# Kernel optimization log

Measured on AMD Instinct MI355X. Metric: run time of the kernel, lower is better.

The kernel has to match this reference:

```python
import jax, jax.numpy as jnp
import numpy as np

WS = 7  # window_size
HEADS = 12
HEAD_DIM = 32
HIDDEN = 384
INNER = HEADS * HEAD_DIM


def _relative_position_index(ws):
    coords = np.stack(np.meshgrid(np.arange(ws), np.arange(ws), indexing='ij'))  # (2, ws, ws)
    flat = coords.reshape(2, -1)  # (2, ws*ws)
    rel = flat[:, :, None] - flat[:, None, :]  # (2, N, N)
    rel = rel.transpose(1, 2, 0).copy()
    rel[:, :, 0] += ws - 1
    rel[:, :, 1] += ws - 1
    rel[:, :, 0] *= 2 * ws - 1
    return rel.sum(-1)  # (N, N) int


def setup_inputs() -> dict:
    key = jax.random.key(0)
    k1, k2, k3, k4, k5 = jax.random.split(key, 5)
    x = jax.random.normal(k1, (32, 56, 56, HIDDEN), dtype=jnp.float32)
    w_qkv = jax.random.normal(k2, (HIDDEN, INNER * 3), dtype=jnp.float32) * (HIDDEN ** -0.5)
    w_out = jax.random.normal(k3, (INNER, HIDDEN), dtype=jnp.float32) * (INNER ** -0.5)
    b_out = jax.random.normal(k4, (HIDDEN,), dtype=jnp.float32) * 0.02
    bias_table = jax.random.normal(k5, ((2 * WS - 1) * (2 * WS - 1), HEADS), dtype=jnp.float32) * 0.02
    return {"x": x, "w_qkv": w_qkv, "w_out": w_out, "b_out": b_out, "bias_table": bias_table}


def _window_attention(x, w_qkv, w_out, b_out, bias_table):
    b, n_h, n_w, _ = x.shape
    ws, h, d = WS, HEADS, HEAD_DIM
    nw_h, nw_w = n_h // ws, n_w // ws
    N = ws * ws

    qkv = x @ w_qkv  # (b, n_h, n_w, 3*inner)
    q, k, v = jnp.split(qkv, 3, axis=-1)

    def to_windows(t):
        # (b, n_h, n_w, h*d) -> (b, h, nw_h*nw_w, ws*ws, d)
        t = t.reshape(b, nw_h, ws, nw_w, ws, h, d)
        t = t.transpose(0, 5, 1, 3, 2, 4, 6)
        return t.reshape(b, h, nw_h * nw_w, N, d)

    q, k, v = map(to_windows, (q, k, v))
    scale = d ** -0.5
    dots = jnp.einsum('bhwid,bhwjd->bhwij', q, k) * scale
    attn = jax.nn.softmax(dots, axis=-1)

    rel_idx = jnp.asarray(_relative_position_index(ws))  # (N, N)
    bias = bias_table[rel_idx.reshape(-1)].reshape(N, N, h)  # gather
    bias = bias.transpose(2, 0, 1)  # (h, N, N)
    # NOTE: faithful to source — bias added AFTER softmax
    attn = attn + bias[None, :, None, :, :]

    out = jnp.einsum('bhwij,bhwjd->bhwid', attn, v)  # (b, h, nw, N, d)
    out = out.reshape(b, h, nw_h, nw_w, ws, ws, d)
    out = out.transpose(0, 2, 4, 3, 5, 1, 6).reshape(b, n_h, n_w, h * d)
    return out @ w_out + b_out


def reference(x, w_qkv, w_out, b_out, bias_table):
    return _window_attention(x, w_qkv, w_out, b_out, bias_table)
```

## Files before the change

### kernel.cpp

```cpp
#include <hip/hip_runtime.h>
#include <hip/hip_bf16.h>
#include <cstdint>

#define TOK 100352
#define HID 384
#define NQKV 1152
#define NHEADS 12
#define HDIM 32

typedef __attribute__((ext_vector_type(8))) short bhalf8;
typedef __attribute__((ext_vector_type(4))) float f32x4;

__device__ __forceinline__ ushort f2bf(float f) {
  uint32_t u = __float_as_uint(f);
  return (ushort)((u + 0x7FFFu + ((u >> 16) & 1u)) >> 16);
}

__device__ __forceinline__ void gload_lds16(const ushort* g, ushort* l) {
  __builtin_amdgcn_global_load_lds(
      (const __attribute__((address_space(1))) unsigned int*)g,
      (__attribute__((address_space(3))) unsigned int*)l, 16, 0, 0);
}

__device__ __forceinline__ uint32_t cvtpk(float a, float b) {
  uint32_t r;
  asm("v_cvt_pk_bf16_f32 %0, %1, %2" : "=v"(r) : "v"(a), "v"(b));
  return r;
}

__global__ __launch_bounds__(256)
void cvt_bf16(const float* __restrict__ in, ushort* __restrict__ out, const int n8) {
  const int i = blockIdx.x * 256 + threadIdx.x;
  if (i >= n8) return;
  const float4 f0 = ((const float4*)in)[(size_t)i * 2];
  const float4 f1 = ((const float4*)in)[(size_t)i * 2 + 1];
  bhalf8 v;
  v[0] = (short)f2bf(f0.x); v[1] = (short)f2bf(f0.y);
  v[2] = (short)f2bf(f0.z); v[3] = (short)f2bf(f0.w);
  v[4] = (short)f2bf(f1.x); v[5] = (short)f2bf(f1.y);
  v[6] = (short)f2bf(f1.z); v[7] = (short)f2bf(f1.w);
  ((bhalf8*)out)[i] = v;
}

__global__ __launch_bounds__(256)
void transpose_cvt(const float* __restrict__ in, ushort* __restrict__ out,
                   const int R, const int C) {
  const int i = blockIdx.x * 256 + threadIdx.x;
  if (i >= R * C) return;
  const int r = i % R, c = i / R;
  out[i] = f2bf(in[(size_t)r * C + c]);
}

__global__ __launch_bounds__(256)
void expand_bias_pad(const float* __restrict__ bt, float* __restrict__ bx) {
  const int i = blockIdx.x * 256 + threadIdx.x;
  if (i >= NHEADS * 49 * 64) return;
  const int head = i / (49 * 64);
  const int rem = i % (49 * 64);
  const int q = rem / 64, k = rem % 64;
  float v = 0.f;
  if (k < 49) {
    const int idx = (q / 7 - k / 7 + 6) * 13 + (q % 7 - k % 7 + 6);
    v = bt[idx * NHEADS + head];
  }
  bx[i] = v;
}

template<bool OUT_F32_BIAS>
__global__ __launch_bounds__(256)
void gemm_bt(const ushort* __restrict__ A, const ushort* __restrict__ Bt,
             const float* __restrict__ bias, void* __restrict__ Cp,
             const int N, const int K, const int nbx)
{
  __shared__ ushort As[128 * 64];
  __shared__ ushort Bs[128 * 64];

  const int tid = threadIdx.x;
  const int lane = tid & 63;
  const int wave = tid >> 6;
  const int wm = wave >> 1, wn = wave & 1;
  const int l15 = lane & 15, l16 = lane >> 4;

  int bid = blockIdx.x;
  const int nwg = gridDim.x;
  if ((nwg & 7) == 0) bid = (bid & 7) * (nwg >> 3) + (bid >> 3);
  const int row0 = (bid / nbx) * 128;
  const int col0 = (bid % nbx) * 128;

  f32x4 acc[4][4] = {};

  for (int ko = 0; ko < K; ko += 64) {
    if (ko) __syncthreads();
    #pragma unroll
    for (int it = 0; it < 4; ++it) {
      const int chunk = it * 4 + wave;
      const int idx = chunk * 64 + lane;
      const int m = idx >> 3;
      const int k8 = (((idx & 7) ^ (m & 7)) * 8);
      gload_lds16(A + (size_t)(row0 + m) * K + ko + k8, &As[chunk * 512]);
      gload_lds16(Bt + (size_t)(col0 + m) * K + ko + k8, &Bs[chunk * 512]);
    }
    __syncthreads();
    #pragma unroll
    for (int kk = 0; kk < 64; kk += 32) {
      bhalf8 af[4], bfr[4];
      #pragma unroll
      for (int f = 0; f < 4; ++f) {
        const int ra = wm * 64 + f * 16 + l15;
        const int rb = wn * 64 + f * 16 + l15;
        const int kb = (kk + l16 * 8) * 2;
        af[f]  = *(const bhalf8*)((const char*)As + ra * 128 + (kb ^ ((ra & 7) << 4)));
        bfr[f] = *(const bhalf8*)((const char*)Bs + rb * 128 + (kb ^ ((rb & 7) << 4)));
      }
      #pragma unroll
      for (int fm = 0; fm < 4; ++fm)
        #pragma unroll
        for (int fn = 0; fn < 4; ++fn)
          acc[fm][fn] = __builtin_amdgcn_mfma_f32_16x16x32_bf16(af[fm], bfr[fn], acc[fm][fn], 0, 0, 0);
    }
  }

  #pragma unroll
  for (int fm = 0; fm < 4; ++fm) {
    const int rb = row0 + wm * 64 + fm * 16 + l16 * 4;
    #pragma unroll
    for (int fn = 0; fn < 4; ++fn) {
      const int cc = col0 + wn * 64 + fn * 16 + l15;
      const float badd = OUT_F32_BIAS ? bias[cc] : 0.f;
      #pragma unroll
      for (int i = 0; i < 4; ++i) {
        const float vv = acc[fm][fn][i] + badd;
        if (OUT_F32_BIAS) ((float*)Cp)[(size_t)(rb + i) * N + cc] = vv;
        else ((ushort*)Cp)[(size_t)(rb + i) * N + cc] = f2bf(vv);
      }
    }
  }
}

__global__ __launch_bounds__(256)
void win_attn4(const ushort* __restrict__ qkv, const float* __restrict__ biasx,
               ushort* __restrict__ attn_out)
{
  __shared__ ushort VtAll[4][32 * 64];
  __shared__ ushort PsAll[4][64 * 64];

  const int tid = threadIdx.x;
  const int lane = tid & 63, wave = tid >> 6;
  const int l15 = lane & 15, l16 = lane >> 4;
  const int gid = blockIdx.x * 4 + wave;
  const int head = gid % NHEADS;
  const int win = gid / NHEADS;
  const int b = win >> 6, wi = (win >> 3) & 7, wj = win & 7;
  char* Vt = (char*)VtAll[wave];
  char* Ps = (char*)PsAll[wave];

  const int base_row = b * 3136 + wi * 7 * 56 + wj * 7;

  #pragma unroll
  for (int it = 0; it < 4; ++it) {
    const int t = lane;
    const int d0 = it * 8;
    bhalf8 v = {0, 0, 0, 0, 0, 0, 0, 0};
    if (t < 49) {
      const size_t off = (size_t)(base_row + (t / 7) * 56 + (t % 7)) * NQKV
                         + 768 + head * HDIM + d0;
      v = *(const bhalf8*)(qkv + off);
    }
    #pragma unroll
    for (int j = 0; j < 8; ++j) {
      const int d = d0 + j;
      const int byteoff = ((d * 64 + t) * 2) ^ ((d & 7) << 4);
      *(ushort*)(Vt + byteoff) = (ushort)v[j];
    }
  }

  bhalf8 qf[4], kf[4];
  #pragma unroll
  for (int f = 0; f < 4; ++f) {
    const int r = f * 16 + l15;
    const int rr = r < 49 ? r : 48;
    const size_t off = (size_t)(base_row + (rr / 7) * 56 + (rr % 7)) * NQKV
                       + head * HDIM + l16 * 8;
    qf[f] = *(const bhalf8*)(qkv + off);
    kf[f] = *(const bhalf8*)(qkv + off + 384);
  }

  const f32x4 fz = {};
  f32x4 s[4][4];
  __builtin_amdgcn_s_setprio(1);
  #pragma unroll
  for (int fm = 0; fm < 4; ++fm)
    #pragma unroll
    for (int fn = 0; fn < 4; ++fn)
      s[fm][fn] = __builtin_amdgcn_mfma_f32_16x16x32_bf16(kf[fm], qf[fn], fz, 0, 0, 0);
  __builtin_amdgcn_s_setprio(0);

  const float scale = 0.17677669529663687f;
  const float* bq = biasx + (size_t)head * (49 * 64);

  #pragma unroll
  for (int fn = 0; fn < 4; ++fn) {
    const int q = fn * 16 + l15;
    const int xr = (q & 7) << 4;
    char* prow = Ps + q * 128;
    if (fn == 3 && l15 != 0) {
      #pragma unroll
      for (int fm = 0; fm < 4; ++fm) {
        const int b0 = (fm * 16 + l16 * 4) * 2;
        *(uint32_t*)(prow + (b0 ^ xr)) = 0u;
        *(uint32_t*)(prow + (b0 ^ xr) + 4) = 0u;
      }
    } else {
      float e[4][4];
      float local = 0.f;
      #pragma unroll
      for (int fm = 0; fm < 3; ++fm)
        #pragma unroll
        for (int i = 0; i < 4; ++i) {
          e[fm][i] = __expf(s[fm][fn][i] * scale);
          local += e[fm][i];
        }
      e[3][0] = e[3][1] = e[3][2] = e[3][3] = 0.f;
      if (l16 == 0) {
        e[3][0] = __expf(s[3][fn][0] * scale);
        local += e[3][0];
      }
      float sum = local + __shfl_xor(local, 16);
      sum += __shfl_xor(sum, 32);
      const float inv = __builtin_amdgcn_rcpf(sum);
      const float* b4p = bq + q * 64;
      #pragma unroll
      for (int fm = 0; fm < 4; ++fm) {
        const int k0 = fm * 16 + l16 * 4;
        const float4 b4 = *(const float4*)(b4p + k0);
        const uint32_t w0 = cvtpk(fmaf(e[fm][0], inv, b4.x),
                                  fmaf(e[fm][1], inv, b4.y));
        const uint32_t w1 = cvtpk(fmaf(e[fm][2], inv, b4.z),
                                  fmaf(e[fm][3], inv, b4.w));
        const int b0 = (k0 * 2) ^ xr;
        *(uint32_t*)(prow + b0) = w0;
        *(uint32_t*)(prow + b0 + 4) = w1;
      }
    }
  }

  f32x4 o[4][2] = {};
  #pragma unroll
  for (int kk = 0; kk < 64; kk += 32) {
    bhalf8 pf[4], vf[2];
    #pragma unroll
    for (int f = 0; f < 4; ++f) {
      const int r = f * 16 + l15;
      pf[f] = *(const bhalf8*)(Ps + (((r * 64 + kk + l16 * 8) * 2) ^ ((r & 7) << 4)));
    }
    #pragma unroll
    for (int f = 0; f < 2; ++f) {
      const int d = f * 16 + l15;
      vf[f] = *(const bhalf8*)(Vt + (((d * 64 + kk + l16 * 8) * 2) ^ ((d & 7) << 4)));
    }
    __builtin_amdgcn_s_setprio(1);
    #pragma unroll
    for (int fm = 0; fm < 4; ++fm)
      #pragma unroll
      for (int fn = 0; fn < 2; ++fn)
        o[fm][fn] = __builtin_amdgcn_mfma_f32_16x16x32_bf16(pf[fm], vf[fn], o[fm][fn], 0, 0, 0);
    __builtin_amdgcn_s_setprio(0);
  }

  #pragma unroll
  for (int fm = 0; fm < 4; ++fm) {
    #pragma unroll
    for (int i = 0; i < 4; ++i) {
      const int r = fm * 16 + l16 * 4 + i;
      if (r < 49) {
        const int grow = base_row + (r / 7) * 56 + (r % 7);
        #pragma unroll
        for (int fn = 0; fn < 2; ++fn) {
          const int d = fn * 16 + l15;
          attn_out[(size_t)grow * HID + head * HDIM + d] = f2bf(o[fm][fn][i]);
        }
      }
    }
  }
}

extern "C" void kernel_launch(void* const* d_in, const int* in_sizes, int n_in,
                              void* d_out, int out_size, void* d_ws, size_t ws_size,
                              hipStream_t stream) {
  const float* x          = (const float*)d_in[0];
  const float* w_qkv      = (const float*)d_in[1];
  const float* w_out      = (const float*)d_in[2];
  const float* b_out      = (const float*)d_in[3];
  const float* bias_table = (const float*)d_in[4];
  float* out = (float*)d_out;

  ushort* xb     = (ushort*)d_ws;
  ushort* qkv    = xb + (size_t)TOK * HID;
  ushort* wqkvT  = qkv + (size_t)TOK * NQKV;
  ushort* woutT  = wqkvT + (size_t)NQKV * HID;
  float*  biasx  = (float*)(woutT + (size_t)HID * HID);
  ushort* attn_o = xb;

  {
    const int n8 = TOK * HID / 8;
    cvt_bf16<<<dim3((n8 + 255) / 256), dim3(256), 0, stream>>>(x, xb, n8);
    transpose_cvt<<<dim3(HID * NQKV / 256), dim3(256), 0, stream>>>(w_qkv, wqkvT, HID, NQKV);
    transpose_cvt<<<dim3(HID * HID / 256), dim3(256), 0, stream>>>(w_out, woutT, HID, HID);
    expand_bias_pad<<<dim3((NHEADS * 49 * 64 + 255) / 256), dim3(256), 0, stream>>>(
        bias_table, biasx);
  }

  gemm_bt<false><<<dim3((NQKV / 128) * (TOK / 128)), dim3(256), 0, stream>>>(
      xb, wqkvT, nullptr, qkv, NQKV, HID, NQKV / 128);

  win_attn4<<<dim3(2048 * NHEADS / 4), dim3(256), 0, stream>>>(qkv, biasx, attn_o);

  gemm_bt<true><<<dim3((HID / 128) * (TOK / 128)), dim3(256), 0, stream>>>(
      attn_o, woutT, b_out, out, HID, HID, HID / 128);
}
```

Baseline: 342.8 us.

## Replace QKV GEMM with 256x128-tile ping-pong pipelined kernel

Adds a dedicated QKV projection kernel that uses 512 threads and 256x128 output tiles. It triple-buffers A and double-buffers B in LDS using direct global-to-LDS loads with XOR swizzle, and interleaves prefetch issue with MFMA phases separated by barriers and priority hints. The goal is to hide global load latency and raise MFMA utilisation compared with the generic 128x128 gemm. In exchange it uses more LDS and registers per block, which may lower occupancy, and its hand-placed waitcnt logic is fragile.

Result: slower. 370.8 us (+8.1%).

```diff
diff --git a/kernel.cpp b/kernel.cpp
--- a/kernel.cpp
+++ b/kernel.cpp
@@ -66,6 +66,146 @@
   bx[i] = v;
 }
 
+__global__ __launch_bounds__(512)
+void gemm1_ph(const ushort* __restrict__ A, const ushort* __restrict__ Bt,
+              ushort* __restrict__ C)
+{
+  __shared__ ushort AL[3][16384];
+  __shared__ ushort BL[2][8192];
+
+  const int tid = threadIdx.x;
+  const int lane = tid & 63, wave = tid >> 6;
+  const int wr = wave >> 1;
+  const int wc = wave & 1;
+  const int l15 = lane & 15, l16 = lane >> 4;
+
+  int bid = blockIdx.x;
+  const int nwg = gridDim.x;
+  bid = (bid & 7) * (nwg >> 3) + (bid >> 3);
+  const int row0 = (bid / 9) * 256;
+  const int col0 = (bid % 9) * 128;
+
+  f32x4 acc[4][4] = {};
+
+  auto issueA = [&](int buf, int ko, int r) {
+    const int idx = r * 512 + tid;
+    const int m = idx >> 3;
+    const int k8 = ((idx & 7) ^ (m & 7)) * 8;
+    gload_lds16(A + (size_t)(row0 + m) * HID + ko + k8,
+                &AL[buf][r * 4096 + wave * 512]);
+  };
+  auto issueB = [&](int buf, int ko, int r) {
+    const int idx = r * 512 + tid;
+    const int m = idx >> 3;
+    const int k8 = ((idx & 7) ^ (m & 7)) * 8;
+    gload_lds16(Bt + (size_t)(col0 + m) * HID + ko + k8,
+                &BL[buf][r * 4096 + wave * 512]);
+  };
+  auto rdA = [&](const ushort* base, int f, int kk) -> bhalf8 {
+    const int ra = wr * 64 + f * 16 + l15;
+    const int kb = (kk + l16 * 8) * 2;
+    return *(const bhalf8*)((const char*)base + ra * 128 + (kb ^ ((ra & 7) << 4)));
+  };
+  auto rdB = [&](const ushort* base, int f, int kk) -> bhalf8 {
+    const int rb = wc * 64 + f * 16 + l15;
+    const int kb = (kk + l16 * 8) * 2;
+    return *(const bhalf8*)((const char*)base + rb * 128 + (kb ^ ((rb & 7) << 4)));
+  };
+
+  const int nt = HID / 64;
+  #pragma unroll
+  for (int r = 0; r < 4; ++r) issueA(0, 0, r);
+  issueB(0, 0, 0); issueB(0, 0, 1);
+  #pragma unroll
+  for (int r = 0; r < 4; ++r) issueA(1, 64, r);
+  asm volatile("s_waitcnt vmcnt(4)" ::: "memory");
+  __builtin_amdgcn_sched_barrier(0);
+  __builtin_amdgcn_s_barrier();
+
+  for (int t = 0; t < nt; ++t) {
+    const ushort* pA = AL[t % 3];
+    const ushort* pB = BL[t & 1];
+    const int abuf = (t + 2) % 3, bbuf = (t + 1) & 1;
+    const bool preA = (t + 2) < nt, preB = (t + 1) < nt;
+    const int koA = (t + 2) * 64, koB = (t + 1) * 64;
+    bhalf8 a0, a1, a2, a3, bfr[4];
+
+    a0 = rdA(pA, 0, 0); a1 = rdA(pA, 1, 0);
+    bfr[0] = rdB(pB, 0, 0); bfr[1] = rdB(pB, 1, 0);
+    bfr[2] = rdB(pB, 2, 0); bfr[3] = rdB(pB, 3, 0);
+    if (preB) { issueB(bbuf, koB, 0); issueB(bbuf, koB, 1); }
+    __builtin_amdgcn_s_barrier();
+    asm volatile("s_waitcnt lgkmcnt(0)" ::: "memory");
+    __builtin_amdgcn_sched_barrier(0);
+    __builtin_amdgcn_s_setprio(1);
+    #pragma unroll
+    for (int fn = 0; fn < 4; ++fn) {
+      acc[0][fn] = __builtin_amdgcn_mfma_f32_16x16x32_bf16(a0, bfr[fn], acc[0][fn], 0, 0, 0);
+      acc[1][fn] = __builtin_amdgcn_mfma_f32_16x16x32_bf16(a1, bfr[fn], acc[1][fn], 0, 0, 0);
+    }
+    __builtin_amdgcn_s_setprio(0);
+    __builtin_amdgcn_s_barrier();
+
+    a2 = rdA(pA, 2, 0); a3 = rdA(pA, 3, 0);
+    if (preA) { issueA(abuf, koA, 0); issueA(abuf, koA, 1); }
+    __builtin_amdgcn_s_barrier();
+    asm volatile("s_waitcnt lgkmcnt(0)" ::: "memory");
+    __builtin_amdgcn_sched_barrier(0);
+    __builtin_amdgcn_s_setprio(1);
+    #pragma unroll
+    for (int fn = 0; fn < 4; ++fn) {
+      acc[2][fn] = __builtin_amdgcn_mfma_f32_16x16x32_bf16(a2, bfr[fn], acc[2][fn], 0, 0, 0);
+      acc[3][fn] = __builtin_amdgcn_mfma_f32_16x16x32_bf16(a3, bfr[fn], acc[3][fn], 0, 0, 0);
+    }
+    __builtin_amdgcn_s_setprio(0);
+    __builtin_amdgcn_s_barrier();
+
+    a0 = rdA(pA, 0, 32); a1 = rdA(pA, 1, 32);
+    bfr[0] = rdB(pB, 0, 32); bfr[1] = rdB(pB, 1, 32);
+    bfr[2] = rdB(pB, 2, 32); bfr[3] = rdB(pB, 3, 32);
+    if (preA) { issueA(abuf, koA, 2); issueA(abuf, koA, 3); }
+    __builtin_amdgcn_s_barrier();
+    asm volatile("s_waitcnt lgkmcnt(0)" ::: "memory");
+    __builtin_amdgcn_sched_barrier(0);
+    __builtin_amdgcn_s_setprio(1);
+    #pragma unroll
+    for (int fn = 0; fn < 4; ++fn) {
+      acc[0][fn] = __builtin_amdgcn_mfma_f32_16x16x32_bf16(a0, bfr[fn], acc[0][fn], 0, 0, 0);
+      acc[1][fn] = __builtin_amdgcn_mfma_f32_16x16x32_bf16(a1, bfr[fn], acc[1][fn], 0, 0, 0);
+    }
+    __builtin_amdgcn_s_setprio(0);
+    __builtin_amdgcn_s_barrier();
+
+    a2 = rdA(pA, 2, 32); a3 = rdA(pA, 3, 32);
+    __builtin_amdgcn_s_barrier();
+    asm volatile("s_waitcnt lgkmcnt(0)" ::: "memory");
+    __builtin_amdgcn_sched_barrier(0);
+    __builtin_amdgcn_s_setprio(1);
+    #pragma unroll
+    for (int fn = 0; fn < 4; ++fn) {
+      acc[2][fn] = __builtin_amdgcn_mfma_f32_16x16x32_bf16(a2, bfr[fn], acc[2][fn], 0, 0, 0);
+      acc[3][fn] = __builtin_amdgcn_mfma_f32_16x16x32_bf16(a3, bfr[fn], acc[3][fn], 0, 0, 0);
+    }
+    __builtin_amdgcn_s_setprio(0);
+    if (preA)      { asm volatile("s_waitcnt vmcnt(4)" ::: "memory"); }
+    else if (preB) { asm volatile("s_waitcnt vmcnt(0)" ::: "memory"); }
+    __builtin_amdgcn_sched_barrier(0);
+    __builtin_amdgcn_s_barrier();
+  }
+
+  #pragma unroll
+  for (int fm = 0; fm < 4; ++fm) {
+    const int rb = row0 + wr * 64 + fm * 16 + l16 * 4;
+    #pragma unroll
+    for (int fn = 0; fn < 4; ++fn) {
+      const int cc = col0 + wc * 64 + fn * 16 + l15;
+      #pragma unroll
+      for (int i = 0; i < 4; ++i)
+        C[(size_t)(rb + i) * NQKV + cc] = f2bf(acc[fm][fn][i]);
+    }
+  }
+}
+
 template<bool OUT_F32_BIAS>
 __global__ __launch_bounds__(256)
 void gemm_bt(const ushort* __restrict__ A, const ushort* __restrict__ Bt,
@@ -310,8 +450,7 @@
         bias_table, biasx);
   }
 
-  gemm_bt<false><<<dim3((NQKV / 128) * (TOK / 128)), dim3(256), 0, stream>>>(
-      xb, wqkvT, nullptr, qkv, NQKV, HID, NQKV / 128);
+  gemm1_ph<<<dim3((TOK / 256) * (NQKV / 128)), dim3(512), 0, stream>>>(xb, wqkvT, qkv);
 
   win_attn4<<<dim3(2048 * NHEADS / 4), dim3(256), 0, stream>>>(qkv, biasx, attn_o);
 
```
